# Optimization experiments

Measured on AMD Instinct MI355X. Metric: run time of the kernel, lower is better.

## Reference

```python
import math
import jax, jax.numpy as jnp
import numpy as np

N_NODES = 50000
N_EDGES = 600000
D = 128          # in_dim == out_dim
T = 4            # num_types
R = 4            # num_relations
H = 8            # n_heads
DK = D // H
MAX_LEN = 240    # RelTemporalEncoding max_len
EPS = 1e-5


def _sinusoid_table(n_hid, max_len):
    pos = jnp.arange(max_len, dtype=jnp.float32)[:, None]
    div = jnp.exp(jnp.arange(0, n_hid, 2, dtype=jnp.float32) * (-math.log(10000.0) / n_hid))
    s = jnp.sin(pos * div) / math.sqrt(n_hid)
    c = jnp.cos(pos * div) / math.sqrt(n_hid)
    emb = jnp.zeros((max_len, n_hid), dtype=jnp.float32)
    emb = emb.at[:, 0::2].set(s).at[:, 1::2].set(c)
    return emb


def setup_inputs() -> dict:
    key = jax.random.key(0)
    ks = jax.random.split(key, 24)
    f32 = jnp.float32
    inp = {
        'node_inp': jax.random.normal(ks[0], (N_NODES, D), dtype=f32),
        'node_type': jax.random.randint(ks[1], (N_NODES,), 0, T),
        'edge_index': jax.random.randint(ks[2], (2, N_EDGES), 0, N_NODES),
        'edge_type': jax.random.randint(ks[3], (N_EDGES,), 0, R),
        'edge_time': jax.random.randint(ks[4], (N_EDGES,), 0, MAX_LEN),
        # per-type Linear weights stored as [T, in, out] (x @ W + b)
        'Wk': jax.random.normal(ks[5], (T, D, D), dtype=f32) * 0.05,
        'bk': jnp.zeros((T, D), dtype=f32),
        'Wq': jax.random.normal(ks[6], (T, D, D), dtype=f32) * 0.05,
        'bq': jnp.zeros((T, D), dtype=f32),
        'Wv': jax.random.normal(ks[7], (T, D, D), dtype=f32) * 0.05,
        'bv': jnp.zeros((T, D), dtype=f32),
        'Wa': jax.random.normal(ks[8], (T, D, D), dtype=f32) * 0.05,
        'ba': jnp.zeros((T, D), dtype=f32),
        'gamma': jnp.ones((T, D), dtype=f32),
        'beta': jnp.zeros((T, D), dtype=f32),
        'rel_pri': jnp.ones((R, H), dtype=f32),
        'rel_att': jax.random.normal(ks[9], (R, H, DK, DK), dtype=f32) * 0.1,
        'rel_msg': jax.random.normal(ks[10], (R, H, DK, DK), dtype=f32) * 0.1,
        'skip': jnp.ones((T,), dtype=f32),
        'rte_W': jax.random.normal(ks[11], (D, D), dtype=f32) * 0.05,
        'rte_b': jnp.zeros((D,), dtype=f32),
    }
    return inp


def _type_proj(x, W, b, types):
    # all-type projection [T, N, D] then gather per-node type (T is small)
    allp = jnp.einsum('ni,tio->tno', x, W) + b[:, None, :]
    return allp[types, jnp.arange(x.shape[0])]


def reference(node_inp, node_type, edge_index, edge_type, edge_time,
              Wk, bk, Wq, bq, Wv, bv, Wa, ba, gamma, beta,
              rel_pri, rel_att, rel_msg, skip, rte_W, rte_b):
    N = node_inp.shape[0]
    E = edge_index.shape[1]
    src, tgt = edge_index[0], edge_index[1]  # j (source) -> i (target)

    # --- RelTemporalEncoding: x + Linear(emb[t]); emb is a fixed sinusoid table
    rte_out = _sinusoid_table(D, MAX_LEN) @ rte_W + rte_b  # [240, D]

    # --- per-node type-specific K/Q/V (linearity: K_t(x + rte) = K_t(x) + rte @ Wk_t)
    k_node = _type_proj(node_inp, Wk, bk, node_type)  # [N, D]
    v_node = _type_proj(node_inp, Wv, bv, node_type)
    q_node = _type_proj(node_inp, Wq, bq, node_type)
    k_rte = jnp.einsum('mi,tio->tmo', rte_out, Wk)  # [T, 240, D] (no bias; already in k_node)
    v_rte = jnp.einsum('mi,tio->tmo', rte_out, Wv)

    stype = node_type[src]
    k_e = (k_node[src] + k_rte[stype, edge_time]).reshape(E, H, DK)
    v_e = (v_node[src] + v_rte[stype, edge_time]).reshape(E, H, DK)
    q_e = q_node[tgt].reshape(E, H, DK)

    # --- per-relation head-wise transforms (R is small, fixed loop)
    k2 = jnp.zeros_like(k_e)
    msg = jnp.zeros_like(v_e)
    for r in range(R):
        sel = (edge_type == r)[:, None, None]
        k2 = jnp.where(sel, jnp.einsum('ehk,hkd->ehd', k_e, rel_att[r]), k2)
        msg = jnp.where(sel, jnp.einsum('ehk,hkd->ehd', v_e, rel_msg[r]), msg)

    logits = (q_e * k2).sum(-1) * rel_pri[edge_type] / math.sqrt(DK)  # [E, H]

    # --- softmax over edges grouped by target node
    m = jax.ops.segment_max(logits, tgt, num_segments=N)
    ex = jnp.exp(logits - m[tgt])
    den = jax.ops.segment_sum(ex, tgt, num_segments=N)
    att = ex / den[tgt]  # [E, H]

    res = (msg * att[..., None]).reshape(E, D)
    aggr = jax.ops.segment_sum(res, tgt, num_segments=N)  # [N, D]

    # --- update: per-type FFN + gated skip + per-type LayerNorm
    a = jax.nn.gelu(aggr, approximate=False)
    trans = _type_proj(a, Wa, ba, node_type)  # dropout p used in eval mode -> identity
    alpha = jax.nn.sigmoid(skip)[node_type][:, None]
    h = trans * alpha + node_inp * (1.0 - alpha)
    mu = h.mean(-1, keepdims=True)
    var = ((h - mu) ** 2).mean(-1, keepdims=True)
    out = (h - mu) / jnp.sqrt(var + EPS) * gamma[node_type] + beta[node_type]
    return out
```

## Files before the change

### kernel.cpp

```cpp
#include <hip/hip_runtime.h>
#include <hip/hip_fp16.h>
#include <math.h>

#define NH 8
#define NT 4
#define NR 4
#define MAXLEN 240

typedef __attribute__((ext_vector_type(8))) short bf16x8;
typedef __attribute__((ext_vector_type(4))) float f32x4;

__device__ __forceinline__ unsigned short f2bf(float x) {
    unsigned u = __float_as_uint(x);
    u += 0x7fffu + ((u >> 16) & 1u);
    return (unsigned short)(u >> 16);
}
__device__ __forceinline__ float bflo(unsigned u) { return __uint_as_float(u << 16); }
__device__ __forceinline__ float bfhi(unsigned u) { return __uint_as_float(u & 0xffff0000u); }
__device__ __forceinline__ unsigned pack2(float a, float b) {
    return (unsigned)f2bf(a) | ((unsigned)f2bf(b) << 16);
}

__device__ __forceinline__ void fp8x4_dec(unsigned w, float* f) {
    unsigned ev = w & 0x00ff00ffu;
    unsigned od = (w >> 8) & 0x00ff00ffu;
    unsigned he = ((ev << 8) & 0x80008000u) | ((ev << 7) & 0x3f803f80u);
    unsigned ho = ((od << 8) & 0x80008000u) | ((od << 7) & 0x3f803f80u);
    __half2 h2e = *reinterpret_cast<__half2*>(&he);
    __half2 h2o = *reinterpret_cast<__half2*>(&ho);
    float2 fe = __half22float2(h2e);
    float2 fo = __half22float2(h2o);
    f[0] = fe.x; f[1] = fo.x; f[2] = fe.y; f[3] = fo.y;
}
__device__ __forceinline__ unsigned char f2fp8(float x) {
    float cl = fminf(fmaxf(x, -448.f), 448.f);
    __half h = __float2half(cl * 0.00390625f);
    unsigned short hr = *reinterpret_cast<unsigned short*>(&h);
    unsigned short rnd = (unsigned short)((hr & 0x7fff) + 0x3f + ((hr >> 7) & 1));
    return (unsigned char)(((rnd >> 7) & 0x7f) | ((hr >> 8) & 0x80));
}

__global__ void zero_kernel(int* deg, int* cursor, int* dcnt, int* dcur, int N) {
    int i = blockIdx.x * blockDim.x + threadIdx.x;
    int stride = gridDim.x * blockDim.x;
    if (i < 256) { dcnt[i] = 0; dcur[i] = 0; }
    for (int j = i; j < N; j += stride) { deg[j] = 0; cursor[j] = 0; }
}

__global__ void deg_kernel(const int* __restrict__ ei, int* __restrict__ deg, int E) {
    int i = blockIdx.x * blockDim.x + threadIdx.x;
    int stride = gridDim.x * blockDim.x;
    for (int e = i; e < E; e += stride) atomicAdd(&deg[ei[E + e]], 1);
}

__global__ __launch_bounds__(256) void histA(const int* __restrict__ ntype,
                                             const int* __restrict__ deg,
                                             int* __restrict__ dcnt, int N) {
    __shared__ int h[256];
    int tid = threadIdx.x;
    h[tid] = 0;
    __syncthreads();
    int i = blockIdx.x * 256 + tid;
    if (i < N) atomicAdd(&h[ntype[i] * 64 + 63 - min(deg[i], 63)], 1);
    __syncthreads();
    if (h[tid]) atomicAdd(&dcnt[tid], h[tid]);
}

__global__ __launch_bounds__(256) void histB(const int* __restrict__ dcnt,
                                             int* __restrict__ dbase) {
    __shared__ int tmp[256];
    int v = dcnt[threadIdx.x];
    tmp[threadIdx.x] = v;
    __syncthreads();
    #pragma unroll
    for (int off = 1; off < 256; off <<= 1) {
        int t = threadIdx.x >= off ? tmp[threadIdx.x - off] : 0;
        __syncthreads();
        tmp[threadIdx.x] += t;
        __syncthreads();
    }
    dbase[threadIdx.x] = tmp[threadIdx.x] - v;
}

__global__ __launch_bounds__(256) void histC(const int* __restrict__ ntype,
                                             const int* __restrict__ deg,
                                             const int* __restrict__ dbase, int* __restrict__ dcur,
                                             int* __restrict__ nlist, int* __restrict__ spos,
                                             int* __restrict__ stype_s, int* __restrict__ deg_s,
                                             int N) {
    __shared__ int h[256];
    __shared__ int bb[256];
    __shared__ int cur[256];
    int tid = threadIdx.x;
    h[tid] = 0; cur[tid] = 0;
    __syncthreads();
    int i = blockIdx.x * 256 + tid;
    int b = -1, t = 0, dg = 0;
    if (i < N) {
        t = ntype[i]; dg = deg[i];
        b = t * 64 + 63 - min(dg, 63);
        atomicAdd(&h[b], 1);
    }
    __syncthreads();
    if (h[tid]) bb[tid] = atomicAdd(&dcur[tid], h[tid]);
    __syncthreads();
    if (i < N) {
        int r = atomicAdd(&cur[b], 1);
        int p = dbase[b] + bb[b] + r;
        nlist[p] = i;
        spos[i] = p;
        stype_s[p] = t;
        deg_s[p] = dg;
    }
}

__global__ __launch_bounds__(256) void scanA(const int* __restrict__ deg, int* __restrict__ excl,
                                             int* __restrict__ bsum, int N) {
    __shared__ int tmp[256];
    int i = blockIdx.x * 256 + threadIdx.x;
    int v = i < N ? deg[i] : 0;
    tmp[threadIdx.x] = v;
    __syncthreads();
    #pragma unroll
    for (int off = 1; off < 256; off <<= 1) {
        int t = threadIdx.x >= off ? tmp[threadIdx.x - off] : 0;
        __syncthreads();
        tmp[threadIdx.x] += t;
        __syncthreads();
    }
    if (i < N) excl[i] = tmp[threadIdx.x] - v;
    if (threadIdx.x == 255) bsum[blockIdx.x] = tmp[255];
}

__global__ __launch_bounds__(256) void scanB(int* __restrict__ bsum, int nb) {
    __shared__ int tmp[256];
    int v = threadIdx.x < nb ? bsum[threadIdx.x] : 0;
    tmp[threadIdx.x] = v;
    __syncthreads();
    #pragma unroll
    for (int off = 1; off < 256; off <<= 1) {
        int t = threadIdx.x >= off ? tmp[threadIdx.x - off] : 0;
        __syncthreads();
        tmp[threadIdx.x] += t;
        __syncthreads();
    }
    if (threadIdx.x < nb) bsum[threadIdx.x] = tmp[threadIdx.x] - v;
}

__global__ void scanC(const int* __restrict__ excl, const int* __restrict__ bsum,
                      int* __restrict__ row_start, int N) {
    int i = blockIdx.x * blockDim.x + threadIdx.x;
    if (i < N) row_start[i] = excl[i] + bsum[i >> 8];
}

__global__ void scatter_kernel(const int* __restrict__ ei, const int* __restrict__ etype,
                               const int* __restrict__ etime, const int* __restrict__ spos,
                               const int* __restrict__ dbase,
                               const int* __restrict__ row_start, int* __restrict__ cursor,
                               unsigned* __restrict__ ebuf, int E) {
    int tb1 = dbase[64], tb2 = dbase[128], tb3 = dbase[192];
    int i = blockIdx.x * blockDim.x + threadIdx.x;
    int stride = gridDim.x * blockDim.x;
    for (int e = i; e < E; e += stride) {
        int sps = spos[ei[e]];
        int spt = spos[ei[E + e]];
        int st = (sps >= tb1) + (sps >= tb2) + (sps >= tb3);
        int pos = atomicAdd(&cursor[spt], 1);
        ebuf[row_start[spt] + pos] =
            (unsigned)sps | ((unsigned)etype[e] << 17) | ((unsigned)etime[e] << 19) | ((unsigned)st << 27);
    }
}

__global__ __launch_bounds__(128) void rte_tables(
    const float* __restrict__ rte_W, const float* __restrict__ rte_b,
    const float* __restrict__ Wk, const float* __restrict__ Wv,
    const float* __restrict__ rel_msg,
    unsigned short* __restrict__ krte_bf, unsigned short* __restrict__ vmrte_bf) {
    int m = blockIdx.x, t = blockIdx.y, d = threadIdx.x;
    __shared__ float emb[128];
    __shared__ float sr[128];
    __shared__ float vr[128];
    int j2 = d & ~1;
    float div = expf((float)j2 * (-9.210340371976184f / 128.f));
    float ang = (float)m * div;
    emb[d] = ((d & 1) ? cosf(ang) : sinf(ang)) * 0.08838834764831845f;
    __syncthreads();
    float ro = rte_b[d];
    #pragma unroll 8
    for (int i = 0; i < 128; ++i) ro += emb[i] * rte_W[i * 128 + d];
    sr[d] = ro;
    __syncthreads();
    float ak = 0.f, av = 0.f;
    for (int i = 0; i < 128; ++i) {
        float rv = sr[i];
        ak += rv * Wk[(t * 128 + i) * 128 + d];
        av += rv * Wv[(t * 128 + i) * 128 + d];
    }
    krte_bf[(size_t)(t * MAXLEN + m) * 128 + d] = f2bf(ak * 0.00390625f);
    vr[d] = av;
    __syncthreads();
    int h = d >> 4, dd = d & 15;
    for (int r = 0; r < NR; ++r) {
        float acc = 0.f;
        #pragma unroll
        for (int k = 0; k < 16; ++k)
            acc += vr[h * 16 + k] * rel_msg[((r * NH + h) * 16 + k) * 16 + dd];
        vmrte_bf[(size_t)((t * 4 + r) * MAXLEN + m) * 128 + d] = f2bf(acc * 0.00390625f);
    }
}

__global__ __launch_bounds__(256) void pack_w9(
    const float* __restrict__ Wk, const float* __restrict__ Wq,
    const float* __restrict__ Wv, const float* __restrict__ Wa,
    const float* __restrict__ bk, const float* __restrict__ bq,
    const float* __restrict__ bv, const float* __restrict__ ba,
    const float* __restrict__ rel_att, const float* __restrict__ rel_msg,
    const float* __restrict__ rel_pri,
    short* __restrict__ PW2, float* __restrict__ PB) {
    if (blockIdx.x >= 320) {
        int bidx = (blockIdx.x - 320) * 256 + threadIdx.x;
        int col = bidx & 127, t = (bidx >> 7) & 3, set = bidx >> 9;
        int h = col >> 4, kk = col & 15;
        float val;
        if (set == 0) val = bk[t * 128 + col];
        else if (set == 9) val = ba[t * 128 + col];
        else if (set <= 4) {
            int r = set - 1;
            float pri = rel_pri[r * NH + h] * 64.f;
            float acc = 0.f;
            #pragma unroll
            for (int dp = 0; dp < 16; ++dp)
                acc += bq[t * 128 + h * 16 + dp] * rel_att[((r * NH + h) * 16 + kk) * 16 + dp];
            val = acc * pri;
        } else {
            int r = set - 5;
            float acc = 0.f;
            #pragma unroll
            for (int kp = 0; kp < 16; ++kp)
                acc += bv[t * 128 + h * 16 + kp] * rel_msg[((r * NH + h) * 16 + kp) * 16 + kk];
            val = acc;
        }
        PB[bidx] = val;
        return;
    }
    int idx = blockIdx.x * 256 + threadIdx.x;
    int lane = idx & 63;
    int ks = (idx >> 6) & 3;
    int ctg = (idx >> 8) & 7;
    int t = (idx >> 11) & 3;
    int set = idx >> 13;
    int col = ctg * 16 + (lane & 15);
    int k0 = ks * 32 + (lane >> 4) * 8;
    int h = col >> 4, kk = col & 15;
    unsigned short o[8];
    if (set == 0 || set == 9) {
        const float* W = (set == 0 ? Wk : Wa) + t * 16384;
        #pragma unroll
        for (int j = 0; j < 8; ++j) o[j] = f2bf(W[(k0 + j) * 128 + col]);
    } else if (set <= 4) {
        int r = set - 1;
        float pri = rel_pri[r * NH + h] * 64.f;
        float Ar[16];
        #pragma unroll
        for (int dp = 0; dp < 16; ++dp)
            Ar[dp] = rel_att[((r * NH + h) * 16 + kk) * 16 + dp] * pri;
        #pragma unroll
        for (int j = 0; j < 8; ++j) {
            const float* wr = Wq + (size_t)(t * 128 + k0 + j) * 128 + h * 16;
            float acc = 0.f;
            #pragma unroll
            for (int dp = 0; dp < 16; ++dp) acc += wr[dp] * Ar[dp];
            o[j] = f2bf(acc);
        }
    } else {
        int r = set - 5;
        float Mc[16];
        #pragma unroll
        for (int kp = 0; kp < 16; ++kp)
            Mc[kp] = rel_msg[((r * NH + h) * 16 + kp) * 16 + kk];
        #pragma unroll
        for (int j = 0; j < 8; ++j) {
            const float* wr = Wv + (size_t)(t * 128 + k0 + j) * 128 + h * 16;
            float acc = 0.f;
            #pragma unroll
            for (int kp = 0; kp < 16; ++kp) acc += wr[kp] * Mc[kp];
            o[j] = f2bf(acc);
        }
    }
    uint4 pk;
    pk.x = (unsigned)o[0] | ((unsigned)o[1] << 16);
    pk.y = (unsigned)o[2] | ((unsigned)o[3] << 16);
    pk.z = (unsigned)o[4] | ((unsigned)o[5] << 16);
    pk.w = (unsigned)o[6] | ((unsigned)o[7] << 16);
    *reinterpret_cast<uint4*>(PW2 + (size_t)idx * 8) = pk;
}

__global__ __launch_bounds__(256, 4) void kqv2(
    const float* __restrict__ x, const int* __restrict__ nlist_,
    const int* __restrict__ stype_s, const short* __restrict__ PW2,
    const float* __restrict__ PB,
    unsigned char* __restrict__ kn8, unsigned short* __restrict__ qa_s,
    unsigned char* __restrict__ vm8, int N) {
    __shared__ short af_l[2][4][64][8];
    __shared__ unsigned char ob8[32 * 256];
    __shared__ int st_l[32];
    const int tid = threadIdx.x;
    const int sp0 = blockIdx.x * 32;
    if (tid < 32) {
        int sp = sp0 + tid;
        st_l[tid] = stype_s[sp < N ? sp : N - 1];
    }
    {
        int i = tid >> 3;
        int d0 = (tid & 7) * 16;
        int sp = sp0 + i;
        int nid = nlist_[sp < N ? sp : N - 1];
        const float* xr = x + (size_t)nid * 128 + d0;
        float4 f0 = *reinterpret_cast<const float4*>(xr);
        float4 f1 = *reinterpret_cast<const float4*>(xr + 4);
        float4 f2 = *reinterpret_cast<const float4*>(xr + 8);
        float4 f3 = *reinterpret_cast<const float4*>(xr + 12);
        int m = i >> 4, rr = i & 15;
        int ks = d0 >> 5;
        int sub = (d0 >> 3) & 3;
        uint4 p0, p1;
        p0.x = pack2(f0.x, f0.y); p0.y = pack2(f0.z, f0.w);
        p0.z = pack2(f1.x, f1.y); p0.w = pack2(f1.z, f1.w);
        p1.x = pack2(f2.x, f2.y); p1.y = pack2(f2.z, f2.w);
        p1.z = pack2(f3.x, f3.y); p1.w = pack2(f3.z, f3.w);
        *reinterpret_cast<uint4*>(&af_l[m][ks][sub * 16 + rr][0]) = p0;
        *reinterpret_cast<uint4*>(&af_l[m][ks][(sub + 1) * 16 + rr][0]) = p1;
    }
    __syncthreads();

    const int lane = tid & 63, w = tid >> 6;
    const int col_l = lane & 15, rowg = lane >> 4;
    const int t0 = st_l[0], t1 = st_l[31];

    bf16x8 afr[2][4];
    #pragma unroll
    for (int m = 0; m < 2; ++m)
        #pragma unroll
        for (int ks = 0; ks < 4; ++ks)
            afr[m][ks] = *reinterpret_cast<const bf16x8*>(&af_l[m][ks][lane][0]);

    for (int set = 0; set < 9; ++set) {
        bool isf8 = (set == 0 || set >= 5);
        for (int t = t0; t <= t1; ++t) {
            #pragma unroll
            for (int c = 0; c < 2; ++c) {
                int ctg = w + c * 4;
                bf16x8 pf[4];
                #pragma unroll
                for (int ks = 0; ks < 4; ++ks)
                    pf[ks] = *reinterpret_cast<const bf16x8*>(
                        PW2 + ((size_t)((((set * 4 + t) * 8 + ctg) * 4 + ks) * 64 + lane)) * 8);
                float bval = PB[(set * 4 + t) * 128 + ctg * 16 + col_l];
                #pragma unroll
                for (int m = 0; m < 2; ++m) {
                    f32x4 acc = {0.f, 0.f, 0.f, 0.f};
                    #pragma unroll
                    for (int ks = 0; ks < 4; ++ks)
                        acc = __builtin_amdgcn_mfma_f32_16x16x32_bf16(afr[m][ks], pf[ks], acc, 0, 0, 0);
                    #pragma unroll
                    for (int j = 0; j < 4; ++j) {
                        int i = m * 16 + rowg * 4 + j;
                        if (st_l[i] == t) {
                            if (isf8)
                                ob8[i * 128 + ctg * 16 + col_l] = f2fp8(acc[j] + bval);
                            else
                                reinterpret_cast<unsigned short*>(ob8)[i * 128 + ctg * 16 + col_l] =
                                    f2bf(acc[j] + bval);
                        }
                    }
                }
            }
        }
        __syncthreads();
        if (isf8) {
            int i = tid >> 3, seg = tid & 7;
            int sp = sp0 + i;
            if (sp < N) {
                unsigned char* dst = (set == 0) ? (kn8 + (size_t)sp * 128)
                                                : (vm8 + ((size_t)sp * 4 + (set - 5)) * 128);
                *reinterpret_cast<uint4*>(dst + seg * 16) =
                    *reinterpret_cast<const uint4*>(&ob8[i * 128 + seg * 16]);
            }
        } else {
            int i = tid >> 3, d0 = (tid & 7) * 16;
            int sp = sp0 + i;
            if (sp < N) {
                unsigned short* dst = qa_s + ((size_t)sp * 4 + (set - 1)) * 128;
                const unsigned short* src = reinterpret_cast<const unsigned short*>(ob8) + i * 128 + d0;
                *reinterpret_cast<uint4*>(dst + d0) = *reinterpret_cast<const uint4*>(src);
                *reinterpret_cast<uint4*>(dst + d0 + 8) = *reinterpret_cast<const uint4*>(src + 8);
            }
        }
        __syncthreads();
    }
}

__global__ __launch_bounds__(256) void fused_edge_attn(
    const unsigned* __restrict__ ebuf, const int* __restrict__ row_start,
    const int* __restrict__ deg_s,
    const unsigned char* __restrict__ kn8, const unsigned short* __restrict__ krte_bf,
    const unsigned short* __restrict__ qa_s, const unsigned char* __restrict__ vm8,
    const unsigned short* __restrict__ vmrte_bf,
    unsigned short* __restrict__ aggr_bf, int N) {
    int sp = blockIdx.x * 16 + (threadIdx.x >> 4);
    int l16 = threadIdx.x & 15;
    if (sp >= N) return;
    uint4 q[4];
    #pragma unroll
    for (int r = 0; r < 4; ++r)
        q[r] = *reinterpret_cast<const uint4*>(qa_s + ((size_t)sp * 4 + r) * 128 + l16 * 8);
    int start = row_start[sp], cnt = deg_s[sp];
    float den = 0.f;
    float acc[8] = {0.f, 0.f, 0.f, 0.f, 0.f, 0.f, 0.f, 0.f};
    for (int i = 0; i < cnt; ++i) {
        unsigned e0 = ebuf[start + i];
        int sps0 = e0 & 0x1ffff, r0 = (e0 >> 17) & 3, tm0 = (e0 >> 19) & 255, st0 = (e0 >> 27) & 3;
        uint2 kv = *reinterpret_cast<const uint2*>(kn8 + (size_t)sps0 * 128 + l16 * 8);
        uint4 kr = *reinterpret_cast<const uint4*>(krte_bf + (size_t)(st0 * MAXLEN + tm0) * 128 + l16 * 8);
        uint2 mv = *reinterpret_cast<const uint2*>(vm8 + ((size_t)sps0 * 4 + r0) * 128 + l16 * 8);
        uint4 mr = *reinterpret_cast<const uint4*>(vmrte_bf + (size_t)((st0 * 4 + r0) * MAXLEN + tm0) * 128 + l16 * 8);
        uint4 qr = q[r0];
        float kf[8], mf[8];
        fp8x4_dec(kv.x, kf); fp8x4_dec(kv.y, kf + 4);
        fp8x4_dec(mv.x, mf); fp8x4_dec(mv.y, mf + 4);
        float p = (kf[0] + bflo(kr.x)) * bflo(qr.x) + (kf[1] + bfhi(kr.x)) * bfhi(qr.x)
                + (kf[2] + bflo(kr.y)) * bflo(qr.y) + (kf[3] + bfhi(kr.y)) * bfhi(qr.y)
                + (kf[4] + bflo(kr.z)) * bflo(qr.z) + (kf[5] + bfhi(kr.z)) * bfhi(qr.z)
                + (kf[6] + bflo(kr.w)) * bflo(qr.w) + (kf[7] + bfhi(kr.w)) * bfhi(qr.w);
        p += __shfl_xor(p, 1);
        float w0 = __expf(p);
        den += w0;
        acc[0] += w0 * (mf[0] + bflo(mr.x));
        acc[1] += w0 * (mf[1] + bfhi(mr.x));
        acc[2] += w0 * (mf[2] + bflo(mr.y));
        acc[3] += w0 * (mf[3] + bfhi(mr.y));
        acc[4] += w0 * (mf[4] + bflo(mr.z));
        acc[5] += w0 * (mf[5] + bfhi(mr.z));
        acc[6] += w0 * (mf[6] + bflo(mr.w));
        acc[7] += w0 * (mf[7] + bfhi(mr.w));
    }
    float inv = den > 0.f ? 256.f / den : 0.f;
    uint4 o;
    o.x = pack2(acc[0] * inv, acc[1] * inv);
    o.y = pack2(acc[2] * inv, acc[3] * inv);
    o.z = pack2(acc[4] * inv, acc[5] * inv);
    o.w = pack2(acc[6] * inv, acc[7] * inv);
    *reinterpret_cast<uint4*>(aggr_bf + (size_t)sp * 128 + l16 * 8) = o;
}

__global__ __launch_bounds__(256, 4) void update_sorted(
    const float* __restrict__ x, const int* __restrict__ nlist_,
    const int* __restrict__ stype_s, const short* __restrict__ PW2,
    const float* __restrict__ PB, const float* __restrict__ gamma,
    const float* __restrict__ beta, const float* __restrict__ skip,
    const unsigned short* __restrict__ aggr_bf, float* __restrict__ out, int N) {
    __shared__ short af_l[2][4][64][8];
    __shared__ float hs[32][128];
    __shared__ int st_l[32];
    __shared__ int nid_l[32];
    const int tid = threadIdx.x;
    const int sp0 = blockIdx.x * 32;
    if (tid < 32) {
        int sp = sp0 + tid;
        int spc = sp < N ? sp : N - 1;
        st_l[tid] = stype_s[spc];
        nid_l[tid] = nlist_[spc];
    }
    {
        int i = tid >> 3;
        int d0 = (tid & 7) * 16;
        int spc = sp0 + i < N ? sp0 + i : N - 1;
        const unsigned short* ar = aggr_bf + (size_t)spc * 128 + d0;
        uint4 v0 = *reinterpret_cast<const uint4*>(ar);
        uint4 v1 = *reinterpret_cast<const uint4*>(ar + 8);
        unsigned vv[8] = {v0.x, v0.y, v0.z, v0.w, v1.x, v1.y, v1.z, v1.w};
        float g[16];
        #pragma unroll
        for (int c = 0; c < 8; ++c) {
            float a0 = bflo(vv[c]), a1 = bfhi(vv[c]);
            g[c * 2 + 0] = 0.5f * a0 * (1.f + erff(a0 * 0.7071067811865476f));
            g[c * 2 + 1] = 0.5f * a1 * (1.f + erff(a1 * 0.7071067811865476f));
        }
        int m = i >> 4, rr = i & 15;
        int ks = d0 >> 5;
        int sub = (d0 >> 3) & 3;
        uint4 p0, p1;
        p0.x = pack2(g[0], g[1]);  p0.y = pack2(g[2], g[3]);
        p0.z = pack2(g[4], g[5]);  p0.w = pack2(g[6], g[7]);
        p1.x = pack2(g[8], g[9]);  p1.y = pack2(g[10], g[11]);
        p1.z = pack2(g[12], g[13]); p1.w = pack2(g[14], g[15]);
        *reinterpret_cast<uint4*>(&af_l[m][ks][sub * 16 + rr][0]) = p0;
        *reinterpret_cast<uint4*>(&af_l[m][ks][(sub + 1) * 16 + rr][0]) = p1;
    }
    __syncthreads();

    const int lane = tid & 63, w = tid >> 6;
    const int col_l = lane & 15, rowg = lane >> 4;
    const int t0 = st_l[0], t1 = st_l[31];

    bf16x8 afr[2][4];
    #pragma unroll
    for (int m = 0; m < 2; ++m)
        #pragma unroll
        for (int ks = 0; ks < 4; ++ks)
            afr[m][ks] = *reinterpret_cast<const bf16x8*>(&af_l[m][ks][lane][0]);

    for (int t = t0; t <= t1; ++t) {
        #pragma unroll
        for (int c = 0; c < 2; ++c) {
            int ctg = w + c * 4;
            bf16x8 pf[4];
            #pragma unroll
            for (int ks = 0; ks < 4; ++ks)
                pf[ks] = *reinterpret_cast<const bf16x8*>(
                    PW2 + ((size_t)((((9 * 4 + t) * 8 + ctg) * 4 + ks) * 64 + lane)) * 8);
            float bval = PB[(9 * 4 + t) * 128 + ctg * 16 + col_l];
            #pragma unroll
            for (int m = 0; m < 2; ++m) {
                f32x4 acc = {0.f, 0.f, 0.f, 0.f};
                #pragma unroll
                for (int ks = 0; ks < 4; ++ks)
                    acc = __builtin_amdgcn_mfma_f32_16x16x32_bf16(afr[m][ks], pf[ks], acc, 0, 0, 0);
                #pragma unroll
                for (int j = 0; j < 4; ++j) {
                    int i = m * 16 + rowg * 4 + j;
                    if (st_l[i] == t)
                        hs[i][ctg * 16 + col_l] = acc[j] + bval;
                }
            }
        }
    }
    __syncthreads();

    {
        int i = tid >> 3;
        int d0 = (tid & 7) * 16;
        int sp = sp0 + i;
        int nid = nid_l[i];
        int t = st_l[i];
        float alpha = 1.f / (1.f + expf(-skip[t]));
        const float* xr = x + (size_t)nid * 128 + d0;
        float hv[16];
        float s1 = 0.f, s2 = 0.f;
        #pragma unroll
        for (int c = 0; c < 4; ++c) {
            float4 xf = *reinterpret_cast<const float4*>(xr + c * 4);
            float4 tf;
            tf.x = hs[i][d0 + c * 4 + 0]; tf.y = hs[i][d0 + c * 4 + 1];
            tf.z = hs[i][d0 + c * 4 + 2]; tf.w = hs[i][d0 + c * 4 + 3];
            hv[c * 4 + 0] = tf.x * alpha + xf.x * (1.f - alpha);
            hv[c * 4 + 1] = tf.y * alpha + xf.y * (1.f - alpha);
            hv[c * 4 + 2] = tf.z * alpha + xf.z * (1.f - alpha);
            hv[c * 4 + 3] = tf.w * alpha + xf.w * (1.f - alpha);
            #pragma unroll
            for (int j = 0; j < 4; ++j) { s1 += hv[c * 4 + j]; s2 += hv[c * 4 + j] * hv[c * 4 + j]; }
        }
        #pragma unroll
        for (int off = 1; off < 8; off <<= 1) {
            s1 += __shfl_xor(s1, off);
            s2 += __shfl_xor(s2, off);
        }
        float mu = s1 * (1.f / 128.f);
        float var = s2 * (1.f / 128.f) - mu * mu;
        float inv = 1.f / sqrtf(var + 1e-5f);
        if (sp < N) {
            float* orow = out + (size_t)nid * 128 + d0;
            const float* gr = gamma + t * 128 + d0;
            const float* br = beta + t * 128 + d0;
            #pragma unroll
            for (int c = 0; c < 4; ++c) {
                float4 gf = *reinterpret_cast<const float4*>(gr + c * 4);
                float4 bf = *reinterpret_cast<const float4*>(br + c * 4);
                float4 of;
                of.x = (hv[c * 4 + 0] - mu) * inv * gf.x + bf.x;
                of.y = (hv[c * 4 + 1] - mu) * inv * gf.y + bf.y;
                of.z = (hv[c * 4 + 2] - mu) * inv * gf.z + bf.z;
                of.w = (hv[c * 4 + 3] - mu) * inv * gf.w + bf.w;
                *reinterpret_cast<float4*>(orow + c * 4) = of;
            }
        }
    }
}

extern "C" void kernel_launch(void* const* d_in, const int* in_sizes, int n_in,
                              void* d_out, int out_size, void* d_ws, size_t ws_size,
                              hipStream_t stream) {
    const float* node_inp = (const float*)d_in[0];
    const int*   node_type = (const int*)d_in[1];
    const int*   edge_index = (const int*)d_in[2];
    const int*   edge_type = (const int*)d_in[3];
    const int*   edge_time = (const int*)d_in[4];
    const float* Wk = (const float*)d_in[5];
    const float* bk = (const float*)d_in[6];
    const float* Wq = (const float*)d_in[7];
    const float* bq = (const float*)d_in[8];
    const float* Wv = (const float*)d_in[9];
    const float* bv = (const float*)d_in[10];
    const float* Wa = (const float*)d_in[11];
    const float* ba = (const float*)d_in[12];
    const float* gamma = (const float*)d_in[13];
    const float* beta = (const float*)d_in[14];
    const float* rel_pri = (const float*)d_in[15];
    const float* rel_att = (const float*)d_in[16];
    const float* rel_msg = (const float*)d_in[17];
    const float* skip = (const float*)d_in[18];
    const float* rte_W = (const float*)d_in[19];
    const float* rte_b = (const float*)d_in[20];

    int N = in_sizes[0] / 128;
    int E = in_sizes[3];

    char* base = (char*)d_ws;
    unsigned short* aggr_bf = (unsigned short*)base;  base += (size_t)N * 128 * 2;
    unsigned char* kn8 = (unsigned char*)base;        base += (size_t)N * 128;
    unsigned char* vm8 = (unsigned char*)base;        base += (size_t)N * 4 * 128;
    unsigned short* qa_s = (unsigned short*)base;     base += (size_t)N * 4 * 128 * 2;
    unsigned short* krte_bf = (unsigned short*)base;  base += (size_t)NT * MAXLEN * 128 * 2;
    unsigned short* vmrte_bf = (unsigned short*)base; base += (size_t)NT * NR * MAXLEN * 128 * 2;
    short* PW2 = (short*)base;                base += (size_t)10 * NT * 128 * 128 * 2;
    float* PB = (float*)base;                 base += (size_t)10 * NT * 128 * 4;
    int* deg = (int*)base;                    base += (size_t)N * 4;
    int* deg_s = (int*)base;                  base += (size_t)N * 4;
    int* cursor = (int*)base;                 base += (size_t)N * 4;
    int* excl = (int*)base;                   base += (size_t)N * 4;
    int* row_start = (int*)base;              base += (size_t)N * 4;
    int* nlist = (int*)base;                  base += (size_t)N * 4;
    int* spos = (int*)base;                   base += (size_t)N * 4;
    int* stype_s = (int*)base;                base += (size_t)N * 4;
    int* bsum = (int*)base;                   base += 256 * 4;
    int* dcnt = (int*)base;                   base += 256 * 4;
    int* dcur = (int*)base;                   base += 256 * 4;
    int* dbase = (int*)base;                  base += 256 * 4;
    base = (char*)(((size_t)base + 15) & ~(size_t)15);
    unsigned* ebuf = (unsigned*)base;         base += (size_t)E * 4;

    int nb = (N + 255) / 256;
    int ng = (N + 255) / 256;

    zero_kernel<<<256, 256, 0, stream>>>(deg, cursor, dcnt, dcur, N);
    deg_kernel<<<1024, 256, 0, stream>>>(edge_index, deg, E);
    histA<<<ng, 256, 0, stream>>>(node_type, deg, dcnt, N);
    histB<<<1, 256, 0, stream>>>(dcnt, dbase);
    histC<<<ng, 256, 0, stream>>>(node_type, deg, dbase, dcur, nlist, spos, stype_s, deg_s, N);
    scanA<<<nb, 256, 0, stream>>>(deg_s, excl, bsum, N);
    scanB<<<1, 256, 0, stream>>>(bsum, nb);
    scanC<<<nb, 256, 0, stream>>>(excl, bsum, row_start, N);
    scatter_kernel<<<1024, 256, 0, stream>>>(edge_index, edge_type, edge_time, spos, dbase,
                                             row_start, cursor, ebuf, E);
    dim3 gt(MAXLEN, NT);
    rte_tables<<<gt, 128, 0, stream>>>(rte_W, rte_b, Wk, Wv, rel_msg, krte_bf, vmrte_bf);
    pack_w9<<<340, 256, 0, stream>>>(Wk, Wq, Wv, Wa, bk, bq, bv, ba,
                                     rel_att, rel_msg, rel_pri, PW2, PB);
    kqv2<<<(N + 31) / 32, 256, 0, stream>>>(node_inp, nlist, stype_s, PW2, PB,
                                            kn8, qa_s, vm8, N);
    fused_edge_attn<<<(N + 15) / 16, 256, 0, stream>>>(ebuf, row_start, deg_s,
                                                       kn8, krte_bf, qa_s, vm8, vmrte_bf,
                                                       aggr_bf, N);
    update_sorted<<<(N + 31) / 32, 256, 0, stream>>>(node_inp, nlist, stype_s, PW2, PB,
                                                     gamma, beta, skip, aggr_bf, (float*)d_out, N);
}
```

Before: 257.0 us.

## Use hardware FP8 conversions, pad LDS staging rows, unroll edge loop by two

Replaces the software FP8 encode/decode with the gfx9 packed FP8 conversion builtins and moves the scale factors (the 1/256 and 64 constants) to match the hardware FP8 range, so the attention kernel decodes with fewer ALU ops. The kqv2 LDS output staging buffer gets padded row strides to cut bank conflicts. The per-node edge loop in fused_edge_attn is unrolled by two so the gathers for two edges are in flight together. It risks numeric differences from the changed FP8 format and scaling, and uses more registers.

New measurement: 234.5 us. 1.1x faster.

```diff
diff --git a/kernel.cpp b/kernel.cpp
--- a/kernel.cpp
+++ b/kernel.cpp
@@ -9,6 +9,13 @@
 
 typedef __attribute__((ext_vector_type(8))) short bf16x8;
 typedef __attribute__((ext_vector_type(4))) float f32x4;
+typedef __attribute__((ext_vector_type(2))) float f32x2;
+
+#if defined(__has_builtin)
+#if __has_builtin(__builtin_amdgcn_cvt_pk_f32_fp8) && __has_builtin(__builtin_amdgcn_cvt_pk_fp8_f32)
+#define HAS_HW_FP8 1
+#endif
+#endif
 
 __device__ __forceinline__ unsigned short f2bf(float x) {
     unsigned u = __float_as_uint(x);
@@ -22,22 +29,35 @@
 }
 
 __device__ __forceinline__ void fp8x4_dec(unsigned w, float* f) {
+#ifdef HAS_HW_FP8
+    f32x2 lo = __builtin_amdgcn_cvt_pk_f32_fp8(w, false);
+    f32x2 hi = __builtin_amdgcn_cvt_pk_f32_fp8(w, true);
+    f[0] = lo[0]; f[1] = lo[1]; f[2] = hi[0]; f[3] = hi[1];
+#else
     unsigned ev = w & 0x00ff00ffu;
     unsigned od = (w >> 8) & 0x00ff00ffu;
-    unsigned he = ((ev << 8) & 0x80008000u) | ((ev << 7) & 0x3f803f80u);
-    unsigned ho = ((od << 8) & 0x80008000u) | ((od << 7) & 0x3f803f80u);
+    unsigned he = (((ev << 8) & 0x80008000u) | ((ev << 7) & 0x3f803f80u)) + 0x04000400u;
+    unsigned ho = (((od << 8) & 0x80008000u) | ((od << 7) & 0x3f803f80u)) + 0x04000400u;
     __half2 h2e = *reinterpret_cast<__half2*>(&he);
     __half2 h2o = *reinterpret_cast<__half2*>(&ho);
     float2 fe = __half22float2(h2e);
     float2 fo = __half22float2(h2o);
     f[0] = fe.x; f[1] = fo.x; f[2] = fe.y; f[3] = fo.y;
-}
-__device__ __forceinline__ unsigned char f2fp8(float x) {
-    float cl = fminf(fmaxf(x, -448.f), 448.f);
-    __half h = __float2half(cl * 0.00390625f);
-    unsigned short hr = *reinterpret_cast<unsigned short*>(&h);
-    unsigned short rnd = (unsigned short)((hr & 0x7fff) + 0x3f + ((hr >> 7) & 1));
-    return (unsigned char)(((rnd >> 7) & 0x7f) | ((hr >> 8) & 0x80));
+#endif
+}
+__device__ __forceinline__ unsigned fp8x2_enc(float a, float b) {
+#ifdef HAS_HW_FP8
+    return (unsigned)__builtin_amdgcn_cvt_pk_fp8_f32(a, b, 0, false) & 0xffffu;
+#else
+    auto enc1 = [](float x) -> unsigned {
+        float cl = fminf(fmaxf(x, -448.f), 448.f);
+        __half h = __float2half(cl * 0.00390625f);
+        unsigned short hr = *reinterpret_cast<unsigned short*>(&h);
+        unsigned short rnd = (unsigned short)((hr & 0x7fff) + 0x3f + ((hr >> 7) & 1));
+        return (unsigned)(((rnd >> 7) & 0x7f) | ((hr >> 8) & 0x80));
+    };
+    return enc1(a) | (enc1(b) << 8);
+#endif
 }
 
 __global__ void zero_kernel(int* deg, int* cursor, int* dcnt, int* dcur, int N) {
@@ -196,7 +216,7 @@
         ak += rv * Wk[(t * 128 + i) * 128 + d];
         av += rv * Wv[(t * 128 + i) * 128 + d];
     }
-    krte_bf[(size_t)(t * MAXLEN + m) * 128 + d] = f2bf(ak * 0.00390625f);
+    krte_bf[(size_t)(t * MAXLEN + m) * 128 + d] = f2bf(ak);
     vr[d] = av;
     __syncthreads();
     int h = d >> 4, dd = d & 15;
@@ -205,7 +225,7 @@
         #pragma unroll
         for (int k = 0; k < 16; ++k)
             acc += vr[h * 16 + k] * rel_msg[((r * NH + h) * 16 + k) * 16 + dd];
-        vmrte_bf[(size_t)((t * 4 + r) * MAXLEN + m) * 128 + d] = f2bf(acc * 0.00390625f);
+        vmrte_bf[(size_t)((t * 4 + r) * MAXLEN + m) * 128 + d] = f2bf(acc);
     }
 }
 
@@ -226,7 +246,7 @@
         else if (set == 9) val = ba[t * 128 + col];
         else if (set <= 4) {
             int r = set - 1;
-            float pri = rel_pri[r * NH + h] * 64.f;
+            float pri = rel_pri[r * NH + h] * 0.25f;
             float acc = 0.f;
             #pragma unroll
             for (int dp = 0; dp < 16; ++dp)
@@ -259,7 +279,7 @@
         for (int j = 0; j < 8; ++j) o[j] = f2bf(W[(k0 + j) * 128 + col]);
     } else if (set <= 4) {
         int r = set - 1;
-        float pri = rel_pri[r * NH + h] * 64.f;
+        float pri = rel_pri[r * NH + h] * 0.25f;
         float Ar[16];
         #pragma unroll
         for (int dp = 0; dp < 16; ++dp)
@@ -294,6 +314,9 @@
     pk.w = (unsigned)o[6] | ((unsigned)o[7] << 16);
     *reinterpret_cast<uint4*>(PW2 + (size_t)idx * 8) = pk;
 }
+
+#define S8 144
+#define S16 136
 
 __global__ __launch_bounds__(256, 4) void kqv2(
     const float* __restrict__ x, const int* __restrict__ nlist_,
@@ -302,8 +325,9 @@
     unsigned char* __restrict__ kn8, unsigned short* __restrict__ qa_s,
     unsigned char* __restrict__ vm8, int N) {
     __shared__ short af_l[2][4][64][8];
-    __shared__ unsigned char ob8[32 * 256];
+    __shared__ unsigned char ob8[32 * 272];
     __shared__ int st_l[32];
+    unsigned short* ob16 = reinterpret_cast<unsigned short*>(ob8);
     const int tid = threadIdx.x;
     const int sp0 = blockIdx.x * 32;
     if (tid < 32) {
@@ -362,15 +386,30 @@
                     #pragma unroll
                     for (int ks = 0; ks < 4; ++ks)
                         acc = __builtin_amdgcn_mfma_f32_16x16x32_bf16(afr[m][ks], pf[ks], acc, 0, 0, 0);
-                    #pragma unroll
-                    for (int j = 0; j < 4; ++j) {
-                        int i = m * 16 + rowg * 4 + j;
-                        if (st_l[i] == t) {
-                            if (isf8)
-                                ob8[i * 128 + ctg * 16 + col_l] = f2fp8(acc[j] + bval);
-                            else
-                                reinterpret_cast<unsigned short*>(ob8)[i * 128 + ctg * 16 + col_l] =
-                                    f2bf(acc[j] + bval);
+                    if (isf8) {
+                        float c0 = fminf(fmaxf(acc[0] + bval, -440.f), 440.f);
+                        float c1 = fminf(fmaxf(acc[1] + bval, -440.f), 440.f);
+                        float c2 = fminf(fmaxf(acc[2] + bval, -440.f), 440.f);
+                        float c3 = fminf(fmaxf(acc[3] + bval, -440.f), 440.f);
+                        unsigned pA = fp8x2_enc(c0, c1);
+                        unsigned pB = fp8x2_enc(c2, c3);
+                        unsigned char by[4];
+                        by[0] = (unsigned char)(pA & 0xff);
+                        by[1] = (unsigned char)((pA >> 8) & 0xff);
+                        by[2] = (unsigned char)(pB & 0xff);
+                        by[3] = (unsigned char)((pB >> 8) & 0xff);
+                        #pragma unroll
+                        for (int j = 0; j < 4; ++j) {
+                            int i = m * 16 + rowg * 4 + j;
+                            if (st_l[i] == t)
+                                ob8[i * S8 + ctg * 16 + col_l] = by[j];
+                        }
+                    } else {
+                        #pragma unroll
+                        for (int j = 0; j < 4; ++j) {
+                            int i = m * 16 + rowg * 4 + j;
+                            if (st_l[i] == t)
+                                ob16[i * S16 + ctg * 16 + col_l] = f2bf(acc[j] + bval);
                         }
                     }
                 }
@@ -384,14 +423,14 @@
                 unsigned char* dst = (set == 0) ? (kn8 + (size_t)sp * 128)
                                                 : (vm8 + ((size_t)sp * 4 + (set - 5)) * 128);
                 *reinterpret_cast<uint4*>(dst + seg * 16) =
-                    *reinterpret_cast<const uint4*>(&ob8[i * 128 + seg * 16]);
+                    *reinterpret_cast<const uint4*>(&ob8[i * S8 + seg * 16]);
             }
         } else {
             int i = tid >> 3, d0 = (tid & 7) * 16;
             int sp = sp0 + i;
             if (sp < N) {
                 unsigned short* dst = qa_s + ((size_t)sp * 4 + (set - 1)) * 128;
-                const unsigned short* src = reinterpret_cast<const unsigned short*>(ob8) + i * 128 + d0;
+                const unsigned short* src = ob16 + i * S16 + d0;
                 *reinterpret_cast<uint4*>(dst + d0) = *reinterpret_cast<const uint4*>(src);
                 *reinterpret_cast<uint4*>(dst + d0 + 8) = *reinterpret_cast<const uint4*>(src + 8);
             }
@@ -417,34 +456,75 @@
     int start = row_start[sp], cnt = deg_s[sp];
     float den = 0.f;
     float acc[8] = {0.f, 0.f, 0.f, 0.f, 0.f, 0.f, 0.f, 0.f};
-    for (int i = 0; i < cnt; ++i) {
+    int i = 0;
+    for (; i + 2 <= cnt; i += 2) {
+        unsigned e0 = ebuf[start + i];
+        unsigned e1 = ebuf[start + i + 1];
+        int sps0 = e0 & 0x1ffff, r0 = (e0 >> 17) & 3, tm0 = (e0 >> 19) & 255, st0 = (e0 >> 27) & 3;
+        int sps1 = e1 & 0x1ffff, r1 = (e1 >> 17) & 3, tm1 = (e1 >> 19) & 255, st1 = (e1 >> 27) & 3;
+        uint2 kv0 = *reinterpret_cast<const uint2*>(kn8 + (size_t)sps0 * 128 + l16 * 8);
+        uint4 kr0 = *reinterpret_cast<const uint4*>(krte_bf + (size_t)(st0 * MAXLEN + tm0) * 128 + l16 * 8);
+        uint2 mv0 = *reinterpret_cast<const uint2*>(vm8 + ((size_t)sps0 * 4 + r0) * 128 + l16 * 8);
+        uint4 mr0 = *reinterpret_cast<const uint4*>(vmrte_bf + (size_t)((st0 * 4 + r0) * MAXLEN + tm0) * 128 + l16 * 8);
+        uint2 kv1 = *reinterpret_cast<const uint2*>(kn8 + (size_t)sps1 * 128 + l16 * 8);
+        uint4 kr1 = *reinterpret_cast<const uint4*>(krte_bf + (size_t)(st1 * MAXLEN + tm1) * 128 + l16 * 8);
+        uint2 mv1 = *reinterpret_cast<const uint2*>(vm8 + ((size_t)sps1 * 4 + r1) * 128 + l16 * 8);
+        uint4 mr1 = *reinterpret_cast<const uint4*>(vmrte_bf + (size_t)((st1 * 4 + r1) * MAXLEN + tm1) * 128 + l16 * 8);
+        float kf0[8], mf0[8], kf1[8], mf1[8];
+        fp8x4_dec(kv0.x, kf0); fp8x4_dec(kv0.y, kf0 + 4);
+        fp8x4_dec(mv0.x, mf0); fp8x4_dec(mv0.y, mf0 + 4);
+        fp8x4_dec(kv1.x, kf1); fp8x4_dec(kv1.y, kf1 + 4);
+        fp8x4_dec(mv1.x, mf1); fp8x4_dec(mv1.y, mf1 + 4);
+        uint4 q0 = q[r0], q1 = q[r1];
+        float p0 = (kf0[0] + bflo(kr0.x)) * bflo(q0.x) + (kf0[1] + bfhi(kr0.x)) * bfhi(q0.x)
+                 + (kf0[2] + bflo(kr0.y)) * bflo(q0.y) + (kf0[3] + bfhi(kr0.y)) * bfhi(q0.y)
+                 + (kf0[4] + bflo(kr0.z)) * bflo(q0.z) + (kf0[5] + bfhi(kr0.z)) * bfhi(q0.z)
+                 + (kf0[6] + bflo(kr0.w)) * bflo(q0.w) + (kf0[7] + bfhi(kr0.w)) * bfhi(q0.w);
+        float p1 = (kf1[0] + bflo(kr1.x)) * bflo(q1.x) + (kf1[1] + bfhi(kr1.x)) * bfhi(q1.x)
+                 + (kf1[2] + bflo(kr1.y)) * bflo(q1.y) + (kf1[3] + bfhi(kr1.y)) * bfhi(q1.y)
+                 + (kf1[4] + bflo(kr1.z)) * bflo(q1.z) + (kf1[5] + bfhi(kr1.z)) * bfhi(q1.z)
+                 + (kf1[6] + bflo(kr1.w)) * bflo(q1.w) + (kf1[7] + bfhi(kr1.w)) * bfhi(q1.w);
+        p0 += __shfl_xor(p0, 1);
+        p1 += __shfl_xor(p1, 1);
+        float w0 = __expf(p0), w1 = __expf(p1);
+        den += w0 + w1;
+        acc[0] += w0 * (mf0[0] + bflo(mr0.x)) + w1 * (mf1[0] + bflo(mr1.x));
+        acc[1] += w0 * (mf0[1] + bfhi(mr0.x)) + w1 * (mf1[1] + bfhi(mr1.x));
+        acc[2] += w0 * (mf0[2] + bflo(mr0.y)) + w1 * (mf1[2] + bflo(mr1.y));
+        acc[3] += w0 * (mf0[3] + bfhi(mr0.y)) + w1 * (mf1[3] + bfhi(mr1.y));
+        acc[4] += w0 * (mf0[4] + bflo(mr0.z)) + w1 * (mf1[4] + bflo(mr1.z));
+        acc[5] += w0 * (mf0[5] + bfhi(mr0.z)) + w1 * (mf1[5] + bfhi(mr1.z));
+        acc[6] += w0 * (mf0[6] + bflo(mr0.w)) + w1 * (mf1[6] + bflo(mr1.w));
+        acc[7] += w0 * (mf0[7] + bfhi(mr0.w)) + w1 * (mf1[7] + bfhi(mr1.w));
+    }
+    if (i < cnt) {
         unsigned e0 = ebuf[start + i];
         int sps0 = e0 & 0x1ffff, r0 = (e0 >> 17) & 3, tm0 = (e0 >> 19) & 255, st0 = (e0 >> 27) & 3;
-        uint2 kv = *reinterpret_cast<const uint2*>(kn8 + (size_t)sps0 * 128 + l16 * 8);
-        uint4 kr = *reinterpret_cast<const uint4*>(krte_bf + (size_t)(st0 * MAXLEN + tm0) * 128 + l16 * 8);
-        uint2 mv = *reinterpret_cast<const uint2*>(vm8 + ((size_t)sps0 * 4 + r0) * 128 + l16 * 8);
-        uint4 mr = *reinterpret_cast<const uint4*>(vmrte_bf + (size_t)((st0 * 4 + r0) * MAXLEN + tm0) * 128 + l16 * 8);
-        uint4 qr = q[r0];
-        float kf[8], mf[8];
-        fp8x4_dec(kv.x, kf); fp8x4_dec(kv.y, kf + 4);
-        fp8x4_dec(mv.x, mf); fp8x4_dec(mv.y, mf + 4);
-        float p = (kf[0] + bflo(kr.x)) * bflo(qr.x) + (kf[1] + bfhi(kr.x)) * bfhi(qr.x)
-                + (kf[2] + bflo(kr.y)) * bflo(qr.y) + (kf[3] + bfhi(kr.y)) * bfhi(qr.y)
-                + (kf[4] + bflo(kr.z)) * bflo(qr.z) + (kf[5] + bfhi(kr.z)) * bfhi(qr.z)
-                + (kf[6] + bflo(kr.w)) * bflo(qr.w) + (kf[7] + bfhi(kr.w)) * bfhi(qr.w);
-        p += __shfl_xor(p, 1);
-        float w0 = __expf(p);
+        uint2 kv0 = *reinterpret_cast<const uint2*>(kn8 + (size_t)sps0 * 128 + l16 * 8);
+        uint4 kr0 = *reinterpret_cast<const uint4*>(krte_bf + (size_t)(st0 * MAXLEN + tm0) * 128 + l16 * 8);
+        uint2 mv0 = *reinterpret_cast<const uint2*>(vm8 + ((size_t)sps0 * 4 + r0) * 128 + l16 * 8);
+        uint4 mr0 = *reinterpret_cast<const uint4*>(vmrte_bf + (size_t)((st0 * 4 + r0) * MAXLEN + tm0) * 128 + l16 * 8);
+        float kf0[8], mf0[8];
+        fp8x4_dec(kv0.x, kf0); fp8x4_dec(kv0.y, kf0 + 4);
+        fp8x4_dec(mv0.x, mf0); fp8x4_dec(mv0.y, mf0 + 4);
+        uint4 q0 = q[r0];
+        float p0 = (kf0[0] + bflo(kr0.x)) * bflo(q0.x) + (kf0[1] + bfhi(kr0.x)) * bfhi(q0.x)
+                 + (kf0[2] + bflo(kr0.y)) * bflo(q0.y) + (kf0[3] + bfhi(kr0.y)) * bfhi(q0.y)
+                 + (kf0[4] + bflo(kr0.z)) * bflo(q0.z) + (kf0[5] + bfhi(kr0.z)) * bfhi(q0.z)
+                 + (kf0[6] + bflo(kr0.w)) * bflo(q0.w) + (kf0[7] + bfhi(kr0.w)) * bfhi(q0.w);
+        p0 += __shfl_xor(p0, 1);
+        float w0 = __expf(p0);
         den += w0;
-        acc[0] += w0 * (mf[0] + bflo(mr.x));
-        acc[1] += w0 * (mf[1] + bfhi(mr.x));
-        acc[2] += w0 * (mf[2] + bflo(mr.y));
-        acc[3] += w0 * (mf[3] + bfhi(mr.y));
-        acc[4] += w0 * (mf[4] + bflo(mr.z));
-        acc[5] += w0 * (mf[5] + bfhi(mr.z));
-        acc[6] += w0 * (mf[6] + bflo(mr.w));
-        acc[7] += w0 * (mf[7] + bfhi(mr.w));
-    }
-    float inv = den > 0.f ? 256.f / den : 0.f;
+        acc[0] += w0 * (mf0[0] + bflo(mr0.x));
+        acc[1] += w0 * (mf0[1] + bfhi(mr0.x));
+        acc[2] += w0 * (mf0[2] + bflo(mr0.y));
+        acc[3] += w0 * (mf0[3] + bfhi(mr0.y));
+        acc[4] += w0 * (mf0[4] + bflo(mr0.z));
+        acc[5] += w0 * (mf0[5] + bfhi(mr0.z));
+        acc[6] += w0 * (mf0[6] + bflo(mr0.w));
+        acc[7] += w0 * (mf0[7] + bfhi(mr0.w));
+    }
+    float inv = den > 0.f ? 1.f / den : 0.f;
     uint4 o;
     o.x = pack2(acc[0] * inv, acc[1] * inv);
     o.y = pack2(acc[2] * inv, acc[3] * inv);
```
